# Optimization experiments

Hardware: AMD Instinct MI355X
Metric: run time of the kernel (lower is better)

## Reference

```python
import jax, jax.numpy as jnp
import numpy as np

B, C, H, W = 4, 16, 320, 640


def _propagate_front(x, g):
    """Linear propagation along leading axis.
    x, g: [L, ...]. out[0] = x[0]; out[i] = x[i]*(1-g[i]) + g[i]*out[i-1].
    """
    def step(prev, xg):
        xr, gr = xg
        out = xr * (1.0 - gr) + gr * prev
        return out, out
    _, ys = jax.lax.scan(step, x[0], (x[1:], g[1:]))
    return jnp.concatenate([x[:1], ys], axis=0)


def _propagate(x, g, axis, reverse):
    xm = jnp.moveaxis(x, axis, 0)
    gm = jnp.moveaxis(g, axis, 0)
    if reverse:
        xm = xm[::-1]
        gm = gm[::-1]
    ym = _propagate_front(xm, gm)
    if reverse:
        ym = ym[::-1]
    return jnp.moveaxis(ym, 0, axis)


def setup_inputs() -> dict:
    key = jax.random.key(0)
    ks = jax.random.split(key, 5)
    shape = (B, C, H, W)
    return {
        "input": jax.random.normal(ks[0], shape, dtype=jnp.float32),
        "g0": jax.random.uniform(ks[1], shape, dtype=jnp.float32),
        "g1": jax.random.uniform(ks[2], shape, dtype=jnp.float32),
        "g2": jax.random.uniform(ks[3], shape, dtype=jnp.float32),
        "g3": jax.random.uniform(ks[4], shape, dtype=jnp.float32),
    }


def reference(input, g0, g1, g2, g3):
    # 4-directional gated recurrent grid propagation, fused by elementwise max.
    r_down = _propagate(input, g0, axis=2, reverse=False)   # top -> bottom over H
    r_up = _propagate(input, g1, axis=2, reverse=True)      # bottom -> top over H
    r_right = _propagate(input, g2, axis=3, reverse=False)  # left -> right over W
    r_left = _propagate(input, g3, axis=3, reverse=True)    # right -> left over W
    return jnp.maximum(jnp.maximum(jnp.maximum(r_down, r_up), r_right), r_left)
```

## Files before the change

### kernel.cpp

```cpp
#include <hip/hip_runtime.h>

constexpr int Bn = 4;
constexpr int Cn = 16;
constexpr int Hn = 320;
constexpr int Wn = 640;
constexpr int NCOL = Bn * Cn * Wn;
constexpr int NROW = Bn * Cn * Hn;

constexpr int HS = 10;
constexpr int NS = 32;
constexpr int CPB = 32;
constexpr int GPW = Wn / CPB;

#define REP10(M) M(0) M(1) M(2) M(3) M(4) M(5) M(6) M(7) M(8) M(9)
#define REP10R(M) M(9) M(8) M(7) M(6) M(5) M(4) M(3) M(2) M(1) M(0)

__global__ __launch_bounds__(1024, 4) void vert_both(
    const float* __restrict__ x, const float* __restrict__ g0,
    const float* __restrict__ g1, float* __restrict__ vm) {
  __shared__ float Ad[NS][CPB], Bd[NS][CPB], Au[NS][CPB], Bu[NS][CPB];
  const int grp = blockIdx.x;
  const int bc = grp / GPW;
  const int w0 = (grp % GPW) * CPB;
  const int s = threadIdx.x >> 5;
  const int l = threadIdx.x & 31;
  const int colbase = bc * (Hn * Wn) + w0 + l;
  const int base = colbase + (s * HS) * Wn;

#define DECL(i) float xl##i, rd##i, pd##i, yu##i, pu##i;
  REP10(DECL)
#undef DECL

  {
    int off = base;
    float yy = 0.0f, pp = 1.0f;
#define DSTEP(i)                                                      \
    {                                                                 \
      xl##i = x[off];                                                 \
      float gv = g0[off];                                             \
      float bb = (s == 0 && i == 0) ? 0.0f : gv;                      \
      yy = fmaf(bb, yy - xl##i, xl##i);                               \
      pp *= bb;                                                       \
      rd##i = yy;                                                     \
      pd##i = pp;                                                     \
      off += Wn;                                                      \
    }
    REP10(DSTEP)
#undef DSTEP
    Ad[s][l] = yy;
    Bd[s][l] = pp;
  }

  {
    int off = base + (HS - 1) * Wn;
    float yy = 0.0f, pp = 1.0f;
#define USTEP(i)                                                      \
    {                                                                 \
      float gv = g1[off];                                             \
      float bb = (s == NS - 1 && i == HS - 1) ? 0.0f : gv;            \
      yy = fmaf(bb, yy - xl##i, xl##i);                               \
      pp *= bb;                                                       \
      yu##i = yy;                                                     \
      pu##i = pp;                                                     \
      off -= Wn;                                                      \
    }
    REP10R(USTEP)
#undef USTEP
    Au[s][l] = yy;
    Bu[s][l] = pp;
  }
  __syncthreads();

  if (s == 0) {
    float c = 0.0f;
#pragma unroll
    for (int ss = 0; ss < NS; ++ss) {
      float a = Ad[ss][l], b = Bd[ss][l];
      Ad[ss][l] = c;
      c = fmaf(b, c, a);
    }
  } else if (s == 2) {
    float c = 0.0f;
#pragma unroll
    for (int ss = NS - 1; ss >= 0; --ss) {
      float a = Au[ss][l], b = Bu[ss][l];
      Au[ss][l] = c;
      c = fmaf(b, c, a);
    }
  }
  __syncthreads();

  {
    const float cd = Ad[s][l];
    const float cu = Au[s][l];
    int off = base;
#define FSTEP(i)                                                      \
    {                                                                 \
      float d = fmaf(pd##i, cd, rd##i);                               \
      float u = fmaf(pu##i, cu, yu##i);                               \
      vm[off] = fmaxf(d, u);                                          \
      off += Wn;                                                      \
    }
    REP10(FSTEP)
#undef FSTEP
  }
}

constexpr int WSEG = 10;

__global__ __launch_bounds__(256) void horiz_final(
    const float* __restrict__ x, const float* __restrict__ g2,
    const float* __restrict__ g3, const float* __restrict__ vm,
    float* __restrict__ out) {
  __shared__ float xs[4 * Wn], rrs[4 * Wn], rls[4 * Wn];
  const int tid = threadIdx.x, wv = tid >> 6, l = tid & 63;
  const size_t rowbase = (size_t)blockIdx.x * 4 * Wn;

  const float4* xg = (const float4*)(x + rowbase);
  const float4* g2g = (const float4*)(g2 + rowbase);
  const float4* g3g = (const float4*)(g3 + rowbase);
  const float4* vm4 = (const float4*)(vm + rowbase);
  float4* xsv = (float4*)xs;
  float4* rrv = (float4*)rrs;
  float4* rlv = (float4*)rls;

  const int i0 = tid, i1 = tid + 256, i2 = tid + 512;
  float4 v0, v1, v2;
  xsv[i0] = xg[i0]; rrv[i0] = g2g[i0]; rlv[i0] = g3g[i0]; v0 = vm4[i0];
  xsv[i1] = xg[i1]; rrv[i1] = g2g[i1]; rlv[i1] = g3g[i1]; v1 = vm4[i1];
  if (i2 < Wn) { xsv[i2] = xg[i2]; rrv[i2] = g2g[i2]; rlv[i2] = g3g[i2]; v2 = vm4[i2]; }
  __syncthreads();

  const int rb = wv * Wn + l * WSEG;
  float xl[WSEG], gl[WSEG], yl[WSEG], pl[WSEG];
#pragma unroll
  for (int i = 0; i < WSEG; ++i) { xl[i] = xs[rb + i]; gl[i] = rrs[rb + i]; }

  {
    float y = 0.0f, p = 1.0f;
#pragma unroll
    for (int i = 0; i < WSEG; ++i) {
      float bb = (l == 0 && i == 0) ? 0.0f : gl[i];
      y = fmaf(bb, y - xl[i], xl[i]);
      p *= bb;
      yl[i] = y; pl[i] = p;
    }
    float A = y, B = p;
#pragma unroll
    for (int off = 1; off < 64; off <<= 1) {
      float Au = __shfl_up(A, off);
      float Bu = __shfl_up(B, off);
      if (l >= off) { A = fmaf(B, Au, A); B *= Bu; }
    }
    float c = __shfl_up(A, 1);
    if (l == 0) c = 0.0f;
#pragma unroll
    for (int i = 0; i < WSEG; ++i) rrs[rb + i] = fmaf(pl[i], c, yl[i]);
  }

#pragma unroll
  for (int i = 0; i < WSEG; ++i) gl[i] = rls[rb + i];
  {
    float y = 0.0f, p = 1.0f;
#pragma unroll
    for (int i = WSEG - 1; i >= 0; --i) {
      float bb = (l == 63 && i == WSEG - 1) ? 0.0f : gl[i];
      y = fmaf(bb, y - xl[i], xl[i]);
      p *= bb;
      yl[i] = y; pl[i] = p;
    }
    float A = y, B = p;
#pragma unroll
    for (int off = 1; off < 64; off <<= 1) {
      float Ad = __shfl_down(A, off);
      float Bd = __shfl_down(B, off);
      if (l + off < 64) { A = fmaf(B, Ad, A); B *= Bd; }
    }
    float c = __shfl_down(A, 1);
    if (l == 63) c = 0.0f;
#pragma unroll
    for (int i = 0; i < WSEG; ++i) rls[rb + i] = fmaf(pl[i], c, yl[i]);
  }
  __syncthreads();

  float4* o4 = (float4*)(out + rowbase);
  {
    float4 a = rrv[i0], b = rlv[i0];
    float4 o;
    o.x = fmaxf(fmaxf(a.x, b.x), v0.x);
    o.y = fmaxf(fmaxf(a.y, b.y), v0.y);
    o.z = fmaxf(fmaxf(a.z, b.z), v0.z);
    o.w = fmaxf(fmaxf(a.w, b.w), v0.w);
    o4[i0] = o;
  }
  {
    float4 a = rrv[i1], b = rlv[i1];
    float4 o;
    o.x = fmaxf(fmaxf(a.x, b.x), v1.x);
    o.y = fmaxf(fmaxf(a.y, b.y), v1.y);
    o.z = fmaxf(fmaxf(a.z, b.z), v1.z);
    o.w = fmaxf(fmaxf(a.w, b.w), v1.w);
    o4[i1] = o;
  }
  if (i2 < Wn) {
    float4 a = rrv[i2], b = rlv[i2];
    float4 o;
    o.x = fmaxf(fmaxf(a.x, b.x), v2.x);
    o.y = fmaxf(fmaxf(a.y, b.y), v2.y);
    o.z = fmaxf(fmaxf(a.z, b.z), v2.z);
    o.w = fmaxf(fmaxf(a.w, b.w), v2.w);
    o4[i2] = o;
  }
}

extern "C" void kernel_launch(void* const* d_in, const int* in_sizes, int n_in,
                              void* d_out, int out_size, void* d_ws,
                              size_t ws_size, hipStream_t stream) {
  const float* x = (const float*)d_in[0];
  const float* g0 = (const float*)d_in[1];
  const float* g1 = (const float*)d_in[2];
  const float* g2 = (const float*)d_in[3];
  const float* g3 = (const float*)d_in[4];
  float* out = (float*)d_out;

  vert_both<<<NCOL / CPB, 1024, 0, stream>>>(x, g0, g1, out);
  horiz_final<<<NROW / 4, 256, 0, stream>>>(x, g2, g3, out, out);
}
```

Baseline: 262.9 us.

## Serialize down/up vertical scans via LDS stash to cut register pressure

The vertical kernel now finishes the downward scan and its carry fixup first, then stashes the down results in a 40KB shared buffer. It reloads x from global for the upward scan instead of keeping it in registers. The aim is fewer live registers per thread, so the compiler can hold more waves. In exchange it adds two extra barriers, a second global read of x, serialized carry scans, and 40KB of LDS, which together with the launch-bounds minimum lowered from 4 to 2 blocks may limit occupancy instead.

```diff
diff --git a/kernel.cpp b/kernel.cpp
--- a/kernel.cpp
+++ b/kernel.cpp
@@ -15,10 +15,11 @@
 #define REP10(M) M(0) M(1) M(2) M(3) M(4) M(5) M(6) M(7) M(8) M(9)
 #define REP10R(M) M(9) M(8) M(7) M(6) M(5) M(4) M(3) M(2) M(1) M(0)
 
-__global__ __launch_bounds__(1024, 4) void vert_both(
+__global__ __launch_bounds__(1024, 2) void vert_both(
     const float* __restrict__ x, const float* __restrict__ g0,
     const float* __restrict__ g1, float* __restrict__ vm) {
-  __shared__ float Ad[NS][CPB], Bd[NS][CPB], Au[NS][CPB], Bu[NS][CPB];
+  __shared__ float As[NS][CPB], Bs[NS][CPB];
+  __shared__ float dstash[NS][HS][CPB];
   const int grp = blockIdx.x;
   const int bc = grp / GPW;
   const int w0 = (grp % GPW) * CPB;
@@ -27,19 +28,18 @@
   const int colbase = bc * (Hn * Wn) + w0 + l;
   const int base = colbase + (s * HS) * Wn;
 
-#define DECL(i) float xl##i, rd##i, pd##i, yu##i, pu##i;
-  REP10(DECL)
-#undef DECL
-
+#define DECLD(i) float rd##i, pd##i;
+  REP10(DECLD)
+#undef DECLD
   {
     int off = base;
     float yy = 0.0f, pp = 1.0f;
 #define DSTEP(i)                                                      \
     {                                                                 \
-      xl##i = x[off];                                                 \
+      float xv = x[off];                                              \
       float gv = g0[off];                                             \
       float bb = (s == 0 && i == 0) ? 0.0f : gv;                      \
-      yy = fmaf(bb, yy - xl##i, xl##i);                               \
+      yy = fmaf(bb, yy - xv, xv);                                     \
       pp *= bb;                                                       \
       rd##i = yy;                                                     \
       pd##i = pp;                                                     \
@@ -47,18 +47,41 @@
     }
     REP10(DSTEP)
 #undef DSTEP
-    Ad[s][l] = yy;
-    Bd[s][l] = pp;
-  }
-
+    As[s][l] = yy;
+    Bs[s][l] = pp;
+  }
+  __syncthreads();
+  if (s == 0) {
+    float c = 0.0f;
+#pragma unroll
+    for (int ss = 0; ss < NS; ++ss) {
+      float a = As[ss][l], b = Bs[ss][l];
+      As[ss][l] = c;
+      c = fmaf(b, c, a);
+    }
+  }
+  __syncthreads();
+
+  {
+    const float cd = As[s][l];
+#define STASH(i) dstash[s][i][l] = fmaf(pd##i, cd, rd##i);
+    REP10(STASH)
+#undef STASH
+  }
+  __syncthreads();
+
+#define DECLU(i) float yu##i, pu##i;
+  REP10(DECLU)
+#undef DECLU
   {
     int off = base + (HS - 1) * Wn;
     float yy = 0.0f, pp = 1.0f;
 #define USTEP(i)                                                      \
     {                                                                 \
+      float xv = x[off];                                              \
       float gv = g1[off];                                             \
       float bb = (s == NS - 1 && i == HS - 1) ? 0.0f : gv;            \
-      yy = fmaf(bb, yy - xl##i, xl##i);                               \
+      yy = fmaf(bb, yy - xv, xv);                                     \
       pp *= bb;                                                       \
       yu##i = yy;                                                     \
       pu##i = pp;                                                     \
@@ -66,42 +89,31 @@
     }
     REP10R(USTEP)
 #undef USTEP
-    Au[s][l] = yy;
-    Bu[s][l] = pp;
-  }
-  __syncthreads();
-
+    As[s][l] = yy;
+    Bs[s][l] = pp;
+  }
+  __syncthreads();
   if (s == 0) {
     float c = 0.0f;
 #pragma unroll
-    for (int ss = 0; ss < NS; ++ss) {
-      float a = Ad[ss][l], b = Bd[ss][l];
-      Ad[ss][l] = c;
+    for (int ss = NS - 1; ss >= 0; --ss) {
+      float a = As[ss][l], b = Bs[ss][l];
+      As[ss][l] = c;
       c = fmaf(b, c, a);
     }
-  } else if (s == 2) {
-    float c = 0.0f;
-#pragma unroll
-    for (int ss = NS - 1; ss >= 0; --ss) {
-      float a = Au[ss][l], b = Bu[ss][l];
-      Au[ss][l] = c;
-      c = fmaf(b, c, a);
-    }
-  }
-  __syncthreads();
-
-  {
-    const float cd = Ad[s][l];
-    const float cu = Au[s][l];
-    int off = base;
+  }
+  __syncthreads();
+
+  {
+    const float cu = As[s][l];
+    int off = base + (HS - 1) * Wn;
 #define FSTEP(i)                                                      \
     {                                                                 \
-      float d = fmaf(pd##i, cd, rd##i);                               \
       float u = fmaf(pu##i, cu, yu##i);                               \
-      vm[off] = fmaxf(d, u);                                          \
-      off += Wn;                                                      \
-    }
-    REP10(FSTEP)
+      vm[off] = fmaxf(dstash[s][i][l], u);                            \
+      off -= Wn;                                                      \
+    }
+    REP10R(FSTEP)
 #undef FSTEP
   }
 }
```

After: 262.1 us. Within noise of the previous version (-0.3%).
